# Performance work log

Hardware: AMD Instinct MI355X
Metric: run time of the kernel (lower is better)

Reference implementation:

```python
import jax, jax.numpy as jnp
import numpy as np

N_EXPERTS = 8
D_IN = 1024
D_OUT = 1024
BATCH = 4096


def setup_inputs() -> dict:
    key = jax.random.key(0)
    k_x, k_w, k_b, k_a = jax.random.split(key, 4)
    xs = jax.random.normal(k_x, (BATCH, D_IN), dtype=jnp.float32)
    mxs = jnp.arange(BATCH, dtype=jnp.int32)  # opaque per-sample metadata, passed through
    actions = jax.random.randint(k_a, (BATCH,), 0, N_EXPERTS, dtype=jnp.int64)
    # Expert parameters: each submodule is Linear(D_IN -> D_OUT)
    W = jax.random.normal(k_w, (N_EXPERTS, D_OUT, D_IN), dtype=jnp.float32) / np.sqrt(D_IN)
    b = jax.random.normal(k_b, (N_EXPERTS, D_OUT), dtype=jnp.float32) * 0.01
    return {"xs": xs, "mxs": mxs, "actions": actions, "W": W, "b": b}


def reference(xs, mxs, actions, W, b):
    # Original: per-sample python loop y_i = submodule[actions[i]](x_i); cat along batch.
    # Vectorized: compute all experts densely (E small), then select per-sample row.
    y_all = jnp.einsum("bj,eij->bei", xs, W) + b[None, :, :]  # [B, E, D_OUT]
    ys = jnp.take_along_axis(y_all, actions[:, None, None].astype(jnp.int32), axis=1)
    ys = jnp.squeeze(ys, axis=1)  # [B, D_OUT]
    return (ys, mxs, actions)
```

## Files before the change

### kernel.cpp

```cpp
#include <hip/hip_runtime.h>

#define BATCH 4096
#define D_IN 1024
#define D_OUT 1024
#define N_EXPERTS 8

#define TK 32
#define MAX_TILES 71
#define MAX_TILES_128 39

#define WS_PERM    0
#define WS_STARTS  4096
#define WS_TILE_E  4112
#define WS_TILE_M  4200
#define WS_NTILES  4288

#define WS_XHI_OFF   32768
#define WS_XLO_OFF   (32768 + 8388608)
#define WS_WHI_OFF   (32768 + 2*8388608)
#define WS_WLO_OFF   (32768 + 2*8388608 + 16777216)
#define WS_NEEDED    (32768 + 2*8388608 + 2*16777216)

typedef __attribute__((ext_vector_type(8))) short short8;
typedef __attribute__((ext_vector_type(4))) float f32x4;

__device__ __forceinline__ void cvt8(const float4 a, const float4 b,
                                     short8& h, short8& l) {
    float f[8] = {a.x, a.y, a.z, a.w, b.x, b.y, b.z, b.w};
#pragma unroll
    for (int i = 0; i < 8; ++i) {
        const unsigned u = __float_as_uint(f[i]);
        h[i] = (short)(u >> 16);
        const float r = f[i] - __uint_as_float(u & 0xffff0000u);
        l[i] = (short)(__float_as_uint(r) >> 16);
    }
}

__global__ __launch_bounds__(256) void prep_kernel(
    const int* __restrict__ actions, const int* __restrict__ mxs,
    const float* __restrict__ xs, const float* __restrict__ W,
    int* __restrict__ ws,
    short* __restrict__ XhiP, short* __restrict__ XloP,
    short* __restrict__ WhiP, short* __restrict__ WloP,
    float* __restrict__ out, int meta_mode, int tm_tile)
{
    const int bid = blockIdx.x;
    const int t = threadIdx.x;

    if (bid == 0) {
        __shared__ int chunkoff[64][N_EXPERTS];
        const int lane = t & 63;
        const int wave = t >> 6;

        for (int it = 0; it < 16; ++it) {
            const int c = wave * 16 + it;
            const int a = actions[c * 64 + lane];
            int myc = 0;
#pragma unroll
            for (int e = 0; e < N_EXPERTS; ++e) {
                const unsigned long long me = __ballot(a == e);
                if (lane == e) myc = (int)__popcll(me);
            }
            if (lane < N_EXPERTS) chunkoff[c][lane] = myc;
        }
        __syncthreads();

        if (wave == 0) {
            int cc0 = chunkoff[lane][0], cc1 = chunkoff[lane][1];
            int cc2 = chunkoff[lane][2], cc3 = chunkoff[lane][3];
            int cc4 = chunkoff[lane][4], cc5 = chunkoff[lane][5];
            int cc6 = chunkoff[lane][6], cc7 = chunkoff[lane][7];
            int tot0, tot1, tot2, tot3, tot4, tot5, tot6, tot7;
            int ex0, ex1, ex2, ex3, ex4, ex5, ex6, ex7;
#define SCAN1(CC, TOT, EX) do {                                   \
            int v = CC;                                           \
            _Pragma("unroll")                                     \
            for (int d = 1; d < 64; d <<= 1) {                    \
                const int u = __shfl_up(v, d, 64);                \
                if (lane >= d) v += u;                            \
            }                                                     \
            TOT = __shfl(v, 63, 64);                              \
            EX = v - CC;                                          \
        } while (0)
            SCAN1(cc0, tot0, ex0); SCAN1(cc1, tot1, ex1);
            SCAN1(cc2, tot2, ex2); SCAN1(cc3, tot3, ex3);
            SCAN1(cc4, tot4, ex4); SCAN1(cc5, tot5, ex5);
            SCAN1(cc6, tot6, ex6); SCAN1(cc7, tot7, ex7);
#undef SCAN1
            const int b0 = 0;
            const int b1 = b0 + tot0, b2 = b1 + tot1, b3 = b2 + tot2;
            const int b4 = b3 + tot3, b5 = b4 + tot4, b6 = b5 + tot5;
            const int b7 = b6 + tot6;
            chunkoff[lane][0] = b0 + ex0; chunkoff[lane][1] = b1 + ex1;
            chunkoff[lane][2] = b2 + ex2; chunkoff[lane][3] = b3 + ex3;
            chunkoff[lane][4] = b4 + ex4; chunkoff[lane][5] = b5 + ex5;
            chunkoff[lane][6] = b6 + ex6; chunkoff[lane][7] = b7 + ex7;
            if (lane == 0) {
                ws[WS_STARTS + 0] = b0; ws[WS_STARTS + 1] = b1;
                ws[WS_STARTS + 2] = b2; ws[WS_STARTS + 3] = b3;
                ws[WS_STARTS + 4] = b4; ws[WS_STARTS + 5] = b5;
                ws[WS_STARTS + 6] = b6; ws[WS_STARTS + 7] = b7;
                ws[WS_STARTS + 8] = BATCH;
                int nt = 0;
                int tots[8] = {tot0, tot1, tot2, tot3, tot4, tot5, tot6, tot7};
#pragma unroll
                for (int e = 0; e < N_EXPERTS; ++e)
                    for (int m0 = 0; m0 < tots[e]; m0 += tm_tile) {
                        ws[WS_TILE_E + nt] = e;
                        ws[WS_TILE_M + nt] = m0;
                        ++nt;
                    }
                ws[WS_NTILES] = nt;
            }
        }
        __syncthreads();

        for (int it = 0; it < 16; ++it) {
            const int c = wave * 16 + it;
            const int i = c * 64 + lane;
            const int a = actions[i];
            unsigned long long msel = 0;
#pragma unroll
            for (int e = 0; e < N_EXPERTS; ++e) {
                const unsigned long long me = __ballot(a == e);
                if (a == e) msel = me;
            }
            const int rank = (int)__popcll(msel & ((1ull << lane) - 1ull));
            const int pos = chunkoff[c][a] + rank;
            ws[WS_PERM + pos] = i;
        }
        return;
    }

    if (bid <= 16) {
        const int i = (bid - 1) * 256 + t;
        if (meta_mode == 2) {
            out[BATCH * D_OUT + i] = (float)mxs[i];
            long long* a64 = (long long*)(out + BATCH * D_OUT + BATCH);
            a64[i] = (long long)actions[i];
        } else if (meta_mode == 1) {
            out[BATCH * D_OUT + i] = (float)mxs[i];
            out[BATCH * D_OUT + BATCH + i] = (float)actions[i];
        }
        return;
    }

    const int g = (bid - 17) * 256 + t;
    if (g < 1048576) {
        const int slot = g & 63;
        const int i2   = (g >> 6) & 7;
        const int blk  = g >> 9;
        const int nt   = blk & 7;
        const int kt   = (blk >> 3) & 31;
        const int e    = blk >> 8;
        const int c    = slot & 15;
        const int j    = slot >> 4;
        const int n    = nt * 128 + i2 * 16 + c;
        const float* p = W + ((size_t)(e << 10) + n) * D_IN + kt * 32 + j * 8;
        const float4 f0 = *(const float4*)p;
        const float4 f1 = *(const float4*)(p + 4);
        short8 h, l;
        cvt8(f0, f1, h, l);
        *(short8*)(WhiP + (size_t)g * 8) = h;
        *(short8*)(WloP + (size_t)g * 8) = l;
    } else {
        const int g2 = g - 1048576;
        const float* p = xs + (size_t)g2 * 8;
        const float4 f0 = *(const float4*)p;
        const float4 f1 = *(const float4*)(p + 4);
        short8 h, l;
        cvt8(f0, f1, h, l);
        *(short8*)(XhiP + (size_t)g2 * 8) = h;
        *(short8*)(XloP + (size_t)g2 * 8) = l;
    }
}

#define TM5 128
#define TN5 128

__global__ __launch_bounds__(512) void moe_gemm_pc(
    const short* __restrict__ Xhi, const short* __restrict__ Xlo,
    const short* __restrict__ Whi, const short* __restrict__ Wlo,
    const float* __restrict__ bias, const int* __restrict__ ws,
    float* __restrict__ out)
{
    const int wid = blockIdx.x;
    const int xcd = wid & 7;
    const int j5  = wid >> 3;
    const int nsl = j5 & 7;
    const int tix = (j5 >> 3) * 8 + xcd;
    if (tix >= ws[WS_NTILES]) return;
    const int e   = ws[WS_TILE_E + tix];
    const int m0  = ws[WS_TILE_M + tix];
    const int s0  = ws[WS_STARTS + e];
    const int cnt = ws[WS_STARTS + e + 1] - s0;
    const int n0  = nsl * TN5;

    __shared__ short Ahi[4][8 * 512];
    __shared__ short Alo[4][8 * 512];
    __shared__ short Bhi[4][8 * 512];
    __shared__ short Blo[4][8 * 512];
    __shared__ int   rows_s[TM5];

    const int t = threadIdx.x;
    if (t < TM5) {
        const int r = m0 + t;
        rows_s[t] = (r < cnt) ? ws[WS_PERM + s0 + r] : -1;
    }
    __syncthreads();

    const int lane = t & 63;
    const int wave = t >> 6;
    const int wm = (wave >> 1) * 32;
    const int wn = (wave & 1) * 64;

    const float zf = 0.f;
    f32x4 acc[2][4];
#pragma unroll
    for (int mi = 0; mi < 2; ++mi)
#pragma unroll
        for (int nj = 0; nj < 4; ++nj)
            acc[mi][nj] = (f32x4){zf, zf, zf, zf};

    const int arow0 = rows_s[wave * 16 + (lane & 15)];
    const int arow  = arow0 < 0 ? 0 : arow0;
    const short* aSrcHi = Xhi + (size_t)arow * D_IN + (lane >> 4) * 8;
    const short* aSrcLo = Xlo + (size_t)arow * D_IN + (lane >> 4) * 8;

    const size_t wBase = ((size_t)e * 256 + (size_t)nsl) * 4096;
    const size_t bo = (size_t)wave * 512 + lane * 8;

#define STAGE(KT, BUF) do {                                                    \
        const int _kt = (KT);                                                  \
        __builtin_amdgcn_global_load_lds(                                      \
            (const __attribute__((address_space(1))) void*)(aSrcHi + _kt * 32),\
            (__attribute__((address_space(3))) void*)&Ahi[BUF][wave * 512],    \
            16, 0, 0);                                                         \
        __builtin_amdgcn_global_load_lds(                                      \
            (const __attribute__((address_space(1))) void*)(aSrcLo + _kt * 32),\
            (__attribute__((address_space(3))) void*)&Alo[BUF][wave * 512],    \
            16, 0, 0);                                                         \
        {                                                                      \
            const size_t _wo = wBase + (size_t)_kt * 32768;                    \
            __builtin_amdgcn_global_load_lds(                                  \
                (const __attribute__((address_space(1))) void*)(Whi + _wo + bo), \
                (__attribute__((address_space(3))) void*)&Bhi[BUF][wave * 512],\
                16, 0, 0);                                                     \
            __builtin_amdgcn_global_load_lds(                                  \
                (const __attribute__((address_space(1))) void*)(Wlo + _wo + bo), \
                (__attribute__((address_space(3))) void*)&Blo[BUF][wave * 512],\
                16, 0, 0);                                                     \
        }                                                                      \
    } while (0)

    const int rds = lane * 8;

#define FRAG_MFMA(BUF) do {                                                  \
        short8 ah[2], al[2], bh[4], bl[4];                                   \
        _Pragma("unroll")                                                    \
        for (int i2 = 0; i2 < 2; ++i2) {                                     \
            const int aoff = ((wm >> 4) + i2) * 512 + rds;                   \
            ah[i2] = *(const short8*)&Ahi[BUF][aoff];                        \
            al[i2] = *(const short8*)&Alo[BUF][aoff];                        \
        }                                                                    \
        _Pragma("unroll")                                                    \
        for (int i2 = 0; i2 < 4; ++i2) {                                     \
            const int boff = ((wn >> 4) + i2) * 512 + rds;                   \
            bh[i2] = *(const short8*)&Bhi[BUF][boff];                        \
            bl[i2] = *(const short8*)&Blo[BUF][boff];                        \
        }                                                                    \
        _Pragma("unroll")                                                    \
        for (int mi = 0; mi < 2; ++mi)                                       \
            _Pragma("unroll")                                                \
            for (int nj = 0; nj < 4; ++nj) {                                 \
                acc[mi][nj] = __builtin_amdgcn_mfma_f32_16x16x32_bf16(ah[mi], bh[nj], acc[mi][nj], 0, 0, 0); \
                acc[mi][nj] = __builtin_amdgcn_mfma_f32_16x16x32_bf16(ah[mi], bl[nj], acc[mi][nj], 0, 0, 0); \
                acc[mi][nj] = __builtin_amdgcn_mfma_f32_16x16x32_bf16(al[mi], bh[nj], acc[mi][nj], 0, 0, 0); \
            }                                                                \
    } while (0)

#define WAIT8_BAR() asm volatile("s_waitcnt vmcnt(8) lgkmcnt(0)\n\ts_barrier" ::: "memory")
#define WAIT4_BAR() asm volatile("s_waitcnt vmcnt(4) lgkmcnt(0)\n\ts_barrier" ::: "memory")
#define WAIT0_BAR() asm volatile("s_waitcnt vmcnt(0) lgkmcnt(0)\n\ts_barrier" ::: "memory")

    STAGE(0, 0);
    STAGE(1, 1);
    STAGE(2, 2);

    int kt = 3;
#pragma unroll 1
    for (int i = 0; i < 7; ++i) {
        WAIT8_BAR(); STAGE(kt,     3); FRAG_MFMA(0);
        WAIT8_BAR(); STAGE(kt + 1, 0); FRAG_MFMA(1);
        WAIT8_BAR(); STAGE(kt + 2, 1); FRAG_MFMA(2);
        WAIT8_BAR(); STAGE(kt + 3, 2); FRAG_MFMA(3);
        kt += 4;
    }
    WAIT8_BAR(); STAGE(31, 3); FRAG_MFMA(0);
    WAIT8_BAR(); FRAG_MFMA(1);
    WAIT4_BAR(); FRAG_MFMA(2);
    WAIT0_BAR(); FRAG_MFMA(3);

#undef STAGE
#undef FRAG_MFMA
#undef WAIT8_BAR
#undef WAIT4_BAR
#undef WAIT0_BAR

    const int cl = lane & 15;
    const int qd = lane >> 4;
    float bv[4];
#pragma unroll
    for (int nj = 0; nj < 4; ++nj)
        bv[nj] = bias[e * D_OUT + n0 + wn + nj * 16 + cl];
#pragma unroll
    for (int mi = 0; mi < 2; ++mi) {
#pragma unroll
        for (int reg = 0; reg < 4; ++reg) {
            const int mloc = wm + mi * 16 + qd * 4 + reg;
            const int r = rows_s[mloc];
            if (r >= 0) {
                float* orow = out + (size_t)r * D_OUT + n0 + wn + cl;
#pragma unroll
                for (int nj = 0; nj < 4; ++nj)
                    orow[nj * 16] = acc[mi][nj][reg] + bv[nj];
            }
        }
    }
}

#define TMF 64
#define TNF 128

__global__ __launch_bounds__(256) void moe_gemm_fb(
    const float* __restrict__ xs, const float* __restrict__ W,
    const float* __restrict__ bias, const int* __restrict__ ws,
    float* __restrict__ out)
{
    const int tix = blockIdx.y;
    if (tix >= ws[WS_NTILES]) return;
    const int e   = ws[WS_TILE_E + tix];
    const int m0  = ws[WS_TILE_M + tix];
    const int s0  = ws[WS_STARTS + e];
    const int cnt = ws[WS_STARTS + e + 1] - s0;
    const int n0  = blockIdx.x * TNF;

    __shared__ short Ahi[2][TMF * TK];
    __shared__ short Alo[2][TMF * TK];
    __shared__ short Bhi[2][TNF * TK];
    __shared__ short Blo[2][TNF * TK];
    __shared__ int   rows_s[TMF];

    const int t = threadIdx.x;
    if (t < TMF) {
        const int r = m0 + t;
        rows_s[t] = (r < cnt) ? ws[WS_PERM + s0 + r] : -1;
    }
    __syncthreads();

    const int lane = t & 63;
    const int wave = t >> 6;
    const int wm = (wave & 1) * 32;
    const int wn = (wave >> 1) * 64;

    const float zf = 0.f;
    f32x4 acc[2][4];
#pragma unroll
    for (int mi = 0; mi < 2; ++mi)
#pragma unroll
        for (int nj = 0; nj < 4; ++nj)
            acc[mi][nj] = (f32x4){zf, zf, zf, zf};

    const float* Wb = W + (size_t)e * (D_OUT * (size_t)D_IN) + (size_t)n0 * D_IN;

    const int j  = t & 3;
    const int rr = t >> 2;

    const int arow = rows_s[rr];
    const float* aptr = (arow >= 0) ? (xs + (size_t)arow * D_IN + j * 8) : nullptr;

    const int slotA   = (j * 16 + (rr & 15)) ^ (j << 1);
    const int aoff_st = (rr >> 4) * 512 + slotA * 8;
    const int boff0   = aoff_st;
    const int boff1   = aoff_st + 4 * 512;

    const float* qb0 = Wb + (size_t)rr * D_IN + j * 8;
    const float* qb1 = Wb + (size_t)(64 + rr) * D_IN + j * 8;

    const int rds = (lane ^ ((lane >> 4) << 1)) * 8;

#define LOAD_SET(A0, A1, B0, B1, B2, B3, KOFF) do {                          \
        const int _k = (KOFF);                                               \
        if (aptr) {                                                          \
            A0 = *(const float4*)(aptr + _k);                                \
            A1 = *(const float4*)(aptr + _k + 4);                            \
        }                                                                    \
        B0 = *(const float4*)(qb0 + _k); B1 = *(const float4*)(qb0 + _k + 4);\
        B2 = *(const float4*)(qb1 + _k); B3 = *(const float4*)(qb1 + _k + 4);\
    } while (0)

#define CVT_STORE_SET(A0, A1, B0, B1, B2, B3, BUF) do {                      \
        short8 _h, _l;                                                       \
        cvt8(A0, A1, _h, _l);                                                \
        *(short8*)&Ahi[BUF][aoff_st] = _h; *(short8*)&Alo[BUF][aoff_st] = _l;\
        cvt8(B0, B1, _h, _l);                                                \
        *(short8*)&Bhi[BUF][boff0] = _h;   *(short8*)&Blo[BUF][boff0] = _l;  \
        cvt8(B2, B3, _h, _l);                                                \
        *(short8*)&Bhi[BUF][boff1] = _h;   *(short8*)&Blo[BUF][boff1] = _l;  \
    } while (0)

#define FRAG_MFMA(BUF) do {                                                  \
        short8 ah[2], al[2], bh[4], bl[4];                                   \
        _Pragma("unroll")                                                    \
        for (int i2 = 0; i2 < 2; ++i2) {                                     \
            const int aoff = ((wm >> 4) + i2) * 512 + rds;                   \
            ah[i2] = *(const short8*)&Ahi[BUF][aoff];                        \
            al[i2] = *(const short8*)&Alo[BUF][aoff];                        \
        }                                                                    \
        _Pragma("unroll")                                                    \
        for (int i2 = 0; i2 < 4; ++i2) {                                     \
            const int boff = ((wn >> 4) + i2) * 512 + rds;                   \
            bh[i2] = *(const short8*)&Bhi[BUF][boff];                        \
            bl[i2] = *(const short8*)&Blo[BUF][boff];                        \
        }                                                                    \
        _Pragma("unroll")                                                    \
        for (int mi = 0; mi < 2; ++mi)                                       \
            _Pragma("unroll")                                                \
            for (int nj = 0; nj < 4; ++nj) {                                 \
                acc[mi][nj] = __builtin_amdgcn_mfma_f32_16x16x32_bf16(ah[mi], bh[nj], acc[mi][nj], 0, 0, 0); \
                acc[mi][nj] = __builtin_amdgcn_mfma_f32_16x16x32_bf16(ah[mi], bl[nj], acc[mi][nj], 0, 0, 0); \
                acc[mi][nj] = __builtin_amdgcn_mfma_f32_16x16x32_bf16(al[mi], bh[nj], acc[mi][nj], 0, 0, 0); \
            }                                                                \
    } while (0)

#define PIPE_BARRIER() asm volatile("s_waitcnt lgkmcnt(0)\n\ts_barrier" ::: "memory")

    float4 ax0 = make_float4(0.f, 0.f, 0.f, 0.f), ax1 = ax0;
    float4 bx0, bx1, bx2, bx3;
    float4 ay0 = make_float4(0.f, 0.f, 0.f, 0.f), ay1 = ay0;
    float4 by0, by1, by2, by3;

    LOAD_SET(ax0, ax1, bx0, bx1, bx2, bx3, 0);
    CVT_STORE_SET(ax0, ax1, bx0, bx1, bx2, bx3, 0);
    LOAD_SET(ax0, ax1, bx0, bx1, bx2, bx3, TK);
    PIPE_BARRIER();

    int ke = 2 * TK;
#pragma unroll 1
    for (int i = 0; i < 15; ++i) {
        {
            LOAD_SET(ay0, ay1, by0, by1, by2, by3, ke);
            FRAG_MFMA(0);
            CVT_STORE_SET(ax0, ax1, bx0, bx1, bx2, bx3, 1);
            PIPE_BARRIER();
        }
        {
            LOAD_SET(ax0, ax1, bx0, bx1, bx2, bx3, ke + TK);
            FRAG_MFMA(1);
            CVT_STORE_SET(ay0, ay1, by0, by1, by2, by3, 0);
            PIPE_BARRIER();
        }
        ke += 2 * TK;
    }
    {
        FRAG_MFMA(0);
        CVT_STORE_SET(ax0, ax1, bx0, bx1, bx2, bx3, 1);
        PIPE_BARRIER();
    }
    {
        FRAG_MFMA(1);
    }

#undef LOAD_SET
#undef CVT_STORE_SET
#undef FRAG_MFMA
#undef PIPE_BARRIER

    const int cl = lane & 15;
    const int qd = lane >> 4;
    float bv[4];
#pragma unroll
    for (int nj = 0; nj < 4; ++nj)
        bv[nj] = bias[e * D_OUT + n0 + wn + nj * 16 + cl];
#pragma unroll
    for (int mi = 0; mi < 2; ++mi) {
#pragma unroll
        for (int reg = 0; reg < 4; ++reg) {
            const int mloc = wm + mi * 16 + qd * 4 + reg;
            const int r = rows_s[mloc];
            if (r >= 0) {
                float* orow = out + (size_t)r * D_OUT + n0 + wn + cl;
#pragma unroll
                for (int nj = 0; nj < 4; ++nj)
                    orow[nj * 16] = acc[mi][nj][reg] + bv[nj];
            }
        }
    }
}

extern "C" void kernel_launch(void* const* d_in, const int* in_sizes, int n_in,
                              void* d_out, int out_size, void* d_ws, size_t ws_size,
                              hipStream_t stream) {
    const float* xs      = (const float*)d_in[0];
    const int*   mxs     = (const int*)d_in[1];
    const int*   actions = (const int*)d_in[2];
    const float* W       = (const float*)d_in[3];
    const float* bias    = (const float*)d_in[4];
    float* out = (float*)d_out;
    int*   ws  = (int*)d_ws;
    char*  wsb = (char*)d_ws;

    short* XhiP = (short*)(wsb + WS_XHI_OFF);
    short* XloP = (short*)(wsb + WS_XLO_OFF);
    short* WhiP = (short*)(wsb + WS_WHI_OFF);
    short* WloP = (short*)(wsb + WS_WLO_OFF);

    const int metaOff = BATCH * D_OUT;
    const int meta_mode = (out_size >= metaOff + 3 * BATCH) ? 2
                        : (out_size >= metaOff + 2 * BATCH) ? 1 : 0;

    const bool big = ws_size >= (size_t)WS_NEEDED;
    const int prep_blocks = big ? (17 + 6144) : 17;
    const int tm_tile = big ? TM5 : TMF;

    prep_kernel<<<prep_blocks, 256, 0, stream>>>(
        actions, mxs, xs, W, ws, XhiP, XloP, WhiP, WloP, out, meta_mode, tm_tile);

    if (big) {
        moe_gemm_pc<<<8 * (MAX_TILES_128 + 1), 512, 0, stream>>>(
            XhiP, XloP, WhiP, WloP, bias, ws, out);
    } else {
        dim3 grid(D_OUT / TNF, MAX_TILES, 1);
        moe_gemm_fb<<<grid, 256, 0, stream>>>(xs, W, bias, ws, out);
    }
}
```

Baseline: 160.3 us.

## Replace LDS-staged 128x128 expert GEMM with direct-register 32-row strip kernel

Replaces the 512-thread LDS-pipelined kernel (128x128 tiles, global_load_lds staging into a 4-stage buffer) with a 256-thread kernel that loads pre-packed bf16 hi/lo fragments straight from global memory into registers, with double-buffered register sets and no LDS or barriers. Tiles become 32-row strips by 256 columns, and jobs are split contiguously across XCDs to balance work. This cuts barrier and LDS traffic and reduces padding waste with smaller row tiles. The cost is less data reuse: each wave refetches its own A rows and B fragments from L2, which raises global memory traffic.

```diff
diff --git a/kernel.cpp b/kernel.cpp
--- a/kernel.cpp
+++ b/kernel.cpp
@@ -7,13 +7,14 @@
 
 #define TK 32
 #define MAX_TILES 71
-#define MAX_TILES_128 39
+#define TSTRIP 32
+#define MAX_STRIPS 136
 
 #define WS_PERM    0
 #define WS_STARTS  4096
 #define WS_TILE_E  4112
-#define WS_TILE_M  4200
-#define WS_NTILES  4288
+#define WS_TILE_M  4280
+#define WS_NTILES  4448
 
 #define WS_XHI_OFF   32768
 #define WS_XLO_OFF   (32768 + 8388608)
@@ -175,35 +176,156 @@
     }
 }
 
-#define TM5 128
-#define TN5 128
-
-__global__ __launch_bounds__(512) void moe_gemm_pc(
+__global__ __launch_bounds__(256, 2) void moe_gemm_dr(
     const short* __restrict__ Xhi, const short* __restrict__ Xlo,
     const short* __restrict__ Whi, const short* __restrict__ Wlo,
     const float* __restrict__ bias, const int* __restrict__ ws,
     float* __restrict__ out)
 {
+    __shared__ int rows_s[TSTRIP];
+
+    const int nstrips = ws[WS_NTILES];
+    const int njobs = nstrips * 4;
     const int wid = blockIdx.x;
     const int xcd = wid & 7;
-    const int j5  = wid >> 3;
-    const int nsl = j5 & 7;
-    const int tix = (j5 >> 3) * 8 + xcd;
+    const int lin = wid >> 3;
+    const int q8 = njobs >> 3, r8 = njobs & 7;
+    const int mylen = (xcd < r8) ? (q8 + 1) : q8;
+    if (lin >= mylen) return;
+    const int job = ((xcd < r8) ? xcd * (q8 + 1)
+                                : r8 * (q8 + 1) + (xcd - r8) * q8) + lin;
+    const int q = job / nstrips;
+    const int s = job - q * nstrips;
+
+    const int e   = ws[WS_TILE_E + s];
+    const int m0  = ws[WS_TILE_M + s];
+    const int s0  = ws[WS_STARTS + e];
+    const int cnt = ws[WS_STARTS + e + 1] - s0;
+
+    const int t = threadIdx.x;
+    if (t < TSTRIP) {
+        const int r = m0 + t;
+        rows_s[t] = (r < cnt) ? ws[WS_PERM + s0 + r] : -1;
+    }
+    __syncthreads();
+
+    const int lane = t & 63;
+    const int wave = t >> 6;
+    const int n0 = q * 256 + wave * 64;
+
+    const float zf = 0.f;
+    f32x4 acc[2][4];
+#pragma unroll
+    for (int mi = 0; mi < 2; ++mi)
+#pragma unroll
+        for (int nj = 0; nj < 4; ++nj)
+            acc[mi][nj] = (f32x4){zf, zf, zf, zf};
+
+    const int fr = lane & 15;
+    const int jo = lane >> 4;
+    int r0 = rows_s[fr];      if (r0 < 0) r0 = 0;
+    int r1 = rows_s[16 + fr]; if (r1 < 0) r1 = 0;
+    const short* aH0 = Xhi + (size_t)r0 * D_IN + jo * 8;
+    const short* aH1 = Xhi + (size_t)r1 * D_IN + jo * 8;
+    const short* aL0 = Xlo + (size_t)r0 * D_IN + jo * 8;
+    const short* aL1 = Xlo + (size_t)r1 * D_IN + jo * 8;
+
+    const size_t wtb = ((size_t)e * 32) * 64 + (size_t)(n0 >> 4);
+    const short* bH = Whi + wtb * 512 + lane * 8;
+    const short* bL = Wlo + wtb * 512 + lane * 8;
+
+#define LOADSET(AH0, AH1, AL0, AL1, B0h, B1h, B2h, B3h, B0l, B1l, B2l, B3l, KT) do { \
+        const int _o = (KT) * 32;                                             \
+        AH0 = *(const short8*)(aH0 + _o);                                     \
+        AH1 = *(const short8*)(aH1 + _o);                                     \
+        AL0 = *(const short8*)(aL0 + _o);                                     \
+        AL1 = *(const short8*)(aL1 + _o);                                     \
+        const short* _bh = bH + (size_t)(KT) * 32768;                         \
+        const short* _bl = bL + (size_t)(KT) * 32768;                         \
+        B0h = *(const short8*)(_bh);        B1h = *(const short8*)(_bh + 512);\
+        B2h = *(const short8*)(_bh + 1024); B3h = *(const short8*)(_bh + 1536);\
+        B0l = *(const short8*)(_bl);        B1l = *(const short8*)(_bl + 512);\
+        B2l = *(const short8*)(_bl + 1024); B3l = *(const short8*)(_bl + 1536);\
+    } while (0)
+
+#define MFMA1(MI, NJ, AH, AL, BH, BL) do {                                   \
+        acc[MI][NJ] = __builtin_amdgcn_mfma_f32_16x16x32_bf16(AH, BH, acc[MI][NJ], 0, 0, 0); \
+        acc[MI][NJ] = __builtin_amdgcn_mfma_f32_16x16x32_bf16(AH, BL, acc[MI][NJ], 0, 0, 0); \
+        acc[MI][NJ] = __builtin_amdgcn_mfma_f32_16x16x32_bf16(AL, BH, acc[MI][NJ], 0, 0, 0); \
+    } while (0)
+
+#define MFMASET(AH0, AH1, AL0, AL1, B0h, B1h, B2h, B3h, B0l, B1l, B2l, B3l) do { \
+        MFMA1(0, 0, AH0, AL0, B0h, B0l); MFMA1(0, 1, AH0, AL0, B1h, B1l);    \
+        MFMA1(0, 2, AH0, AL0, B2h, B2l); MFMA1(0, 3, AH0, AL0, B3h, B3l);    \
+        MFMA1(1, 0, AH1, AL1, B0h, B0l); MFMA1(1, 1, AH1, AL1, B1h, B1l);    \
+        MFMA1(1, 2, AH1, AL1, B2h, B2l); MFMA1(1, 3, AH1, AL1, B3h, B3l);    \
+    } while (0)
+
+    short8 xah0, xah1, xal0, xal1, xb0h, xb1h, xb2h, xb3h, xb0l, xb1l, xb2l, xb3l;
+    short8 yah0, yah1, yal0, yal1, yb0h, yb1h, yb2h, yb3h, yb0l, yb1l, yb2l, yb3l;
+
+    LOADSET(xah0, xah1, xal0, xal1, xb0h, xb1h, xb2h, xb3h, xb0l, xb1l, xb2l, xb3l, 0);
+#pragma unroll 1
+    for (int i = 0; i < 15; ++i) {
+        LOADSET(yah0, yah1, yal0, yal1, yb0h, yb1h, yb2h, yb3h, yb0l, yb1l, yb2l, yb3l, 2 * i + 1);
+        MFMASET(xah0, xah1, xal0, xal1, xb0h, xb1h, xb2h, xb3h, xb0l, xb1l, xb2l, xb3l);
+        LOADSET(xah0, xah1, xal0, xal1, xb0h, xb1h, xb2h, xb3h, xb0l, xb1l, xb2l, xb3l, 2 * i + 2);
+        MFMASET(yah0, yah1, yal0, yal1, yb0h, yb1h, yb2h, yb3h, yb0l, yb1l, yb2l, yb3l);
+    }
+    LOADSET(yah0, yah1, yal0, yal1, yb0h, yb1h, yb2h, yb3h, yb0l, yb1l, yb2l, yb3l, 31);
+    MFMASET(xah0, xah1, xal0, xal1, xb0h, xb1h, xb2h, xb3h, xb0l, xb1l, xb2l, xb3l);
+    MFMASET(yah0, yah1, yal0, yal1, yb0h, yb1h, yb2h, yb3h, yb0l, yb1l, yb2l, yb3l);
+
+#undef LOADSET
+#undef MFMA1
+#undef MFMASET
+
+    const int cl = lane & 15;
+    const int qd = lane >> 4;
+    float bv[4];
+#pragma unroll
+    for (int nj = 0; nj < 4; ++nj)
+        bv[nj] = bias[e * D_OUT + n0 + nj * 16 + cl];
+#pragma unroll
+    for (int mi = 0; mi < 2; ++mi) {
+#pragma unroll
+        for (int reg = 0; reg < 4; ++reg) {
+            const int mloc = mi * 16 + qd * 4 + reg;
+            const int r = rows_s[mloc];
+            if (r >= 0) {
+                float* orow = out + (size_t)r * D_OUT + n0 + cl;
+#pragma unroll
+                for (int nj = 0; nj < 4; ++nj)
+                    orow[nj * 16] = acc[mi][nj][reg] + bv[nj];
+            }
+        }
+    }
+}
+
+#define TMF 64
+#define TNF 128
+
+__global__ __launch_bounds__(256) void moe_gemm_fb(
+    const float* __restrict__ xs, const float* __restrict__ W,
+    const float* __restrict__ bias, const int* __restrict__ ws,
+    float* __restrict__ out)
+{
+    const int tix = blockIdx.y;
     if (tix >= ws[WS_NTILES]) return;
     const int e   = ws[WS_TILE_E + tix];
     const int m0  = ws[WS_TILE_M + tix];
     const int s0  = ws[WS_STARTS + e];
     const int cnt = ws[WS_STARTS + e + 1] - s0;
-    const int n0  = nsl * TN5;
-
-    __shared__ short Ahi[4][8 * 512];
-    __shared__ short Alo[4][8 * 512];
-    __shared__ short Bhi[4][8 * 512];
-    __shared__ short Blo[4][8 * 512];
-    __shared__ int   rows_s[TM5];
+    const int n0  = blockIdx.x * TNF;
+
+    __shared__ short Ahi[2][TMF * TK];
+    __shared__ short Alo[2][TMF * TK];
+    __shared__ short Bhi[2][TNF * TK];
+    __shared__ short Blo[2][TNF * TK];
+    __shared__ int   rows_s[TMF];
 
     const int t = threadIdx.x;
-    if (t < TM5) {
+    if (t < TMF) {
         const int r = m0 + t;
         rows_s[t] = (r < cnt) ? ws[WS_PERM + s0 + r] : -1;
     }
@@ -211,8 +333,8 @@
 
     const int lane = t & 63;
     const int wave = t >> 6;
-    const int wm = (wave >> 1) * 32;
-    const int wn = (wave & 1) * 64;
+    const int wm = (wave & 1) * 32;
+    const int wn = (wave >> 1) * 64;
 
     const float zf = 0.f;
     f32x4 acc[2][4];
@@ -222,38 +344,43 @@
         for (int nj = 0; nj < 4; ++nj)
             acc[mi][nj] = (f32x4){zf, zf, zf, zf};
 
-    const int arow0 = rows_s[wave * 16 + (lane & 15)];
-    const int arow  = arow0 < 0 ? 0 : arow0;
-    const short* aSrcHi = Xhi + (size_t)arow * D_IN + (lane >> 4) * 8;
-    const short* aSrcLo = Xlo + (size_t)arow * D_IN + (lane >> 4) * 8;
-
-    const size_t wBase = ((size_t)e * 256 + (size_t)nsl) * 4096;
-    const size_t bo = (size_t)wave * 512 + lane * 8;
-
-#define STAGE(KT, BUF) do {                                                    \
-        const int _kt = (KT);                                                  \
-        __builtin_amdgcn_global_load_lds(                                      \
-            (const __attribute__((address_space(1))) void*)(aSrcHi + _kt * 32),\
-            (__attribute__((address_space(3))) void*)&Ahi[BUF][wave * 512],    \
-            16, 0, 0);                                                         \
-        __builtin_amdgcn_global_load_lds(                                      \
-            (const __attribute__((address_space(1))) void*)(aSrcLo + _kt * 32),\
-            (__attribute__((address_space(3))) void*)&Alo[BUF][wave * 512],    \
-            16, 0, 0);                                                         \
-        {                                                                      \
-            const size_t _wo = wBase + (size_t)_kt * 32768;                    \
-            __builtin_amdgcn_global_load_lds(                                  \
-                (const __attribute__((address_space(1))) void*)(Whi + _wo + bo), \
-                (__attribute__((address_space(3))) void*)&Bhi[BUF][wave * 512],\
-                16, 0, 0);                                                     \
-            __builtin_amdgcn_global_load_lds(                                  \
-                (const __attribute__((address_space(1))) void*)(Wlo + _wo + bo), \
-                (__attribute__((address_space(3))) void*)&Blo[BUF][wave * 512],\
-                16, 0, 0);                                                     \
-        }                                                                      \
+    const float* Wb = W + (size_t)e * (D_OUT * (size_t)D_IN) + (size_t)n0 * D_IN;
+
+    const int j  = t & 3;
+    const int rr = t >> 2;
+
+    const int arow = rows_s[rr];
+    const float* aptr = (arow >= 0) ? (xs + (size_t)arow * D_IN + j * 8) : nullptr;
+
+    const int slotA   = (j * 16 + (rr & 15)) ^ (j << 1);
+    const int aoff_st = (rr >> 4) * 512 + slotA * 8;
+    const int boff0   = aoff_st;
+    const int boff1   = aoff_st + 4 * 512;
+
+    const float* qb0 = Wb + (size_t)rr * D_IN + j * 8;
+    const float* qb1 = Wb + (size_t)(64 + rr) * D_IN + j * 8;
+
+    const int rds = (lane ^ ((lane >> 4) << 1)) * 8;
+
+#define LOAD_SET(A0, A1, B0, B1, B2, B3, KOFF) do {                          \
+        const int _k = (KOFF);                                               \
+        if (aptr) {                                                          \
+            A0 = *(const float4*)(aptr + _k);                                \
+            A1 = *(const float4*)(aptr + _k + 4);                            \
+        }                                                                    \
+        B0 = *(const float4*)(qb0 + _k); B1 = *(const float4*)(qb0 + _k + 4);\
+        B2 = *(const float4*)(qb1 + _k); B3 = *(const float4*)(qb1 + _k + 4);\
     } while (0)
 
-    const int rds = lane * 8;
+#define CVT_STORE_SET(A0, A1, B0, B1, B2, B3, BUF) do {                      \
+        short8 _h, _l;                                                       \
+        cvt8(A0, A1, _h, _l);                                                \
+        *(short8*)&Ahi[BUF][aoff_st] = _h; *(short8*)&Alo[BUF][aoff_st] = _l;\
+        cvt8(B0, B1, _h, _l);                                                \
+        *(short8*)&Bhi[BUF][boff0] = _h;   *(short8*)&Blo[BUF][boff0] = _l;  \
+        cvt8(B2, B3, _h, _l);                                                \
+        *(short8*)&Bhi[BUF][boff1] = _h;   *(short8*)&Blo[BUF][boff1] = _l;  \
+    } while (0)
 
 #define FRAG_MFMA(BUF) do {                                                  \
         short8 ah[2], al[2], bh[4], bl[4];                                   \
@@ -279,160 +406,6 @@
             }                                                                \
     } while (0)
 
-#define WAIT8_BAR() asm volatile("s_waitcnt vmcnt(8) lgkmcnt(0)\n\ts_barrier" ::: "memory")
-#define WAIT4_BAR() asm volatile("s_waitcnt vmcnt(4) lgkmcnt(0)\n\ts_barrier" ::: "memory")
-#define WAIT0_BAR() asm volatile("s_waitcnt vmcnt(0) lgkmcnt(0)\n\ts_barrier" ::: "memory")
-
-    STAGE(0, 0);
-    STAGE(1, 1);
-    STAGE(2, 2);
-
-    int kt = 3;
-#pragma unroll 1
-    for (int i = 0; i < 7; ++i) {
-        WAIT8_BAR(); STAGE(kt,     3); FRAG_MFMA(0);
-        WAIT8_BAR(); STAGE(kt + 1, 0); FRAG_MFMA(1);
-        WAIT8_BAR(); STAGE(kt + 2, 1); FRAG_MFMA(2);
-        WAIT8_BAR(); STAGE(kt + 3, 2); FRAG_MFMA(3);
-        kt += 4;
-    }
-    WAIT8_BAR(); STAGE(31, 3); FRAG_MFMA(0);
-    WAIT8_BAR(); FRAG_MFMA(1);
-    WAIT4_BAR(); FRAG_MFMA(2);
-    WAIT0_BAR(); FRAG_MFMA(3);
-
-#undef STAGE
-#undef FRAG_MFMA
-#undef WAIT8_BAR
-#undef WAIT4_BAR
-#undef WAIT0_BAR
-
-    const int cl = lane & 15;
-    const int qd = lane >> 4;
-    float bv[4];
-#pragma unroll
-    for (int nj = 0; nj < 4; ++nj)
-        bv[nj] = bias[e * D_OUT + n0 + wn + nj * 16 + cl];
-#pragma unroll
-    for (int mi = 0; mi < 2; ++mi) {
-#pragma unroll
-        for (int reg = 0; reg < 4; ++reg) {
-            const int mloc = wm + mi * 16 + qd * 4 + reg;
-            const int r = rows_s[mloc];
-            if (r >= 0) {
-                float* orow = out + (size_t)r * D_OUT + n0 + wn + cl;
-#pragma unroll
-                for (int nj = 0; nj < 4; ++nj)
-                    orow[nj * 16] = acc[mi][nj][reg] + bv[nj];
-            }
-        }
-    }
-}
-
-#define TMF 64
-#define TNF 128
-
-__global__ __launch_bounds__(256) void moe_gemm_fb(
-    const float* __restrict__ xs, const float* __restrict__ W,
-    const float* __restrict__ bias, const int* __restrict__ ws,
-    float* __restrict__ out)
-{
-    const int tix = blockIdx.y;
-    if (tix >= ws[WS_NTILES]) return;
-    const int e   = ws[WS_TILE_E + tix];
-    const int m0  = ws[WS_TILE_M + tix];
-    const int s0  = ws[WS_STARTS + e];
-    const int cnt = ws[WS_STARTS + e + 1] - s0;
-    const int n0  = blockIdx.x * TNF;
-
-    __shared__ short Ahi[2][TMF * TK];
-    __shared__ short Alo[2][TMF * TK];
-    __shared__ short Bhi[2][TNF * TK];
-    __shared__ short Blo[2][TNF * TK];
-    __shared__ int   rows_s[TMF];
-
-    const int t = threadIdx.x;
-    if (t < TMF) {
-        const int r = m0 + t;
-        rows_s[t] = (r < cnt) ? ws[WS_PERM + s0 + r] : -1;
-    }
-    __syncthreads();
-
-    const int lane = t & 63;
-    const int wave = t >> 6;
-    const int wm = (wave & 1) * 32;
-    const int wn = (wave >> 1) * 64;
-
-    const float zf = 0.f;
-    f32x4 acc[2][4];
-#pragma unroll
-    for (int mi = 0; mi < 2; ++mi)
-#pragma unroll
-        for (int nj = 0; nj < 4; ++nj)
-            acc[mi][nj] = (f32x4){zf, zf, zf, zf};
-
-    const float* Wb = W + (size_t)e * (D_OUT * (size_t)D_IN) + (size_t)n0 * D_IN;
-
-    const int j  = t & 3;
-    const int rr = t >> 2;
-
-    const int arow = rows_s[rr];
-    const float* aptr = (arow >= 0) ? (xs + (size_t)arow * D_IN + j * 8) : nullptr;
-
-    const int slotA   = (j * 16 + (rr & 15)) ^ (j << 1);
-    const int aoff_st = (rr >> 4) * 512 + slotA * 8;
-    const int boff0   = aoff_st;
-    const int boff1   = aoff_st + 4 * 512;
-
-    const float* qb0 = Wb + (size_t)rr * D_IN + j * 8;
-    const float* qb1 = Wb + (size_t)(64 + rr) * D_IN + j * 8;
-
-    const int rds = (lane ^ ((lane >> 4) << 1)) * 8;
-
-#define LOAD_SET(A0, A1, B0, B1, B2, B3, KOFF) do {                          \
-        const int _k = (KOFF);                                               \
-        if (aptr) {                                                          \
-            A0 = *(const float4*)(aptr + _k);                                \
-            A1 = *(const float4*)(aptr + _k + 4);                            \
-        }                                                                    \
-        B0 = *(const float4*)(qb0 + _k); B1 = *(const float4*)(qb0 + _k + 4);\
-        B2 = *(const float4*)(qb1 + _k); B3 = *(const float4*)(qb1 + _k + 4);\
-    } while (0)
-
-#define CVT_STORE_SET(A0, A1, B0, B1, B2, B3, BUF) do {                      \
-        short8 _h, _l;                                                       \
-        cvt8(A0, A1, _h, _l);                                                \
-        *(short8*)&Ahi[BUF][aoff_st] = _h; *(short8*)&Alo[BUF][aoff_st] = _l;\
-        cvt8(B0, B1, _h, _l);                                                \
-        *(short8*)&Bhi[BUF][boff0] = _h;   *(short8*)&Blo[BUF][boff0] = _l;  \
-        cvt8(B2, B3, _h, _l);                                                \
-        *(short8*)&Bhi[BUF][boff1] = _h;   *(short8*)&Blo[BUF][boff1] = _l;  \
-    } while (0)
-
-#define FRAG_MFMA(BUF) do {                                                  \
-        short8 ah[2], al[2], bh[4], bl[4];                                   \
-        _Pragma("unroll")                                                    \
-        for (int i2 = 0; i2 < 2; ++i2) {                                     \
-            const int aoff = ((wm >> 4) + i2) * 512 + rds;                   \
-            ah[i2] = *(const short8*)&Ahi[BUF][aoff];                        \
-            al[i2] = *(const short8*)&Alo[BUF][aoff];                        \
-        }                                                                    \
-        _Pragma("unroll")                                                    \
-        for (int i2 = 0; i2 < 4; ++i2) {                                     \
-            const int boff = ((wn >> 4) + i2) * 512 + rds;                   \
-            bh[i2] = *(const short8*)&Bhi[BUF][boff];                        \
-            bl[i2] = *(const short8*)&Blo[BUF][boff];                        \
-        }                                                                    \
-        _Pragma("unroll")                                                    \
-        for (int mi = 0; mi < 2; ++mi)                                       \
-            _Pragma("unroll")                                                \
-            for (int nj = 0; nj < 4; ++nj) {                                 \
-                acc[mi][nj] = __builtin_amdgcn_mfma_f32_16x16x32_bf16(ah[mi], bh[nj], acc[mi][nj], 0, 0, 0); \
-                acc[mi][nj] = __builtin_amdgcn_mfma_f32_16x16x32_bf16(ah[mi], bl[nj], acc[mi][nj], 0, 0, 0); \
-                acc[mi][nj] = __builtin_amdgcn_mfma_f32_16x16x32_bf16(al[mi], bh[nj], acc[mi][nj], 0, 0, 0); \
-            }                                                                \
-    } while (0)
-
 #define PIPE_BARRIER() asm volatile("s_waitcnt lgkmcnt(0)\n\ts_barrier" ::: "memory")
 
     float4 ax0 = make_float4(0.f, 0.f, 0.f, 0.f), ax1 = ax0;
@@ -521,13 +494,13 @@
 
     const bool big = ws_size >= (size_t)WS_NEEDED;
     const int prep_blocks = big ? (17 + 6144) : 17;
-    const int tm_tile = big ? TM5 : TMF;
+    const int tm_tile = big ? TSTRIP : TMF;
 
     prep_kernel<<<prep_blocks, 256, 0, stream>>>(
         actions, mxs, xs, W, ws, XhiP, XloP, WhiP, WloP, out, meta_mode, tm_tile);
 
     if (big) {
-        moe_gemm_pc<<<8 * (MAX_TILES_128 + 1), 512, 0, stream>>>(
+        moe_gemm_dr<<<4 * MAX_STRIPS, 256, 0, stream>>>(
             XhiP, XloP, WhiP, WloP, bias, ws, out);
     } else {
         dim3 grid(D_OUT / TNF, MAX_TILES, 1);
```

Result: slower. 176.0 us (+9.8%).

## Load gathered A fragments directly into registers, stage only weights through LDS

Applied to the files above, without the earlier changes.

The A-operand (gathered input rows, hi/lo bf16 split) is now loaded straight from global memory into registers with double-buffered register sets, and only the weight tiles go through async global-to-LDS copies. This removes the A-side LDS buffers and the LDS reads for A fragments, halving shared memory use and cutting LDS traffic. Launch bounds now request 4 blocks per SM, and the workspace tile-table offsets are widened. The trade-offs are higher register pressure, uncoalesced per-row global loads for A, and a barrier placed inside each compute step.

```diff
diff --git a/kernel.cpp b/kernel.cpp
--- a/kernel.cpp
+++ b/kernel.cpp
@@ -12,8 +12,8 @@
 #define WS_PERM    0
 #define WS_STARTS  4096
 #define WS_TILE_E  4112
-#define WS_TILE_M  4200
-#define WS_NTILES  4288
+#define WS_TILE_M  4280
+#define WS_NTILES  4448
 
 #define WS_XHI_OFF   32768
 #define WS_XLO_OFF   (32768 + 8388608)
@@ -178,7 +178,7 @@
 #define TM5 128
 #define TN5 128
 
-__global__ __launch_bounds__(512) void moe_gemm_pc(
+__global__ __launch_bounds__(512, 4) void moe_gemm_pc(
     const short* __restrict__ Xhi, const short* __restrict__ Xlo,
     const short* __restrict__ Whi, const short* __restrict__ Wlo,
     const float* __restrict__ bias, const int* __restrict__ ws,
@@ -196,8 +196,6 @@
     const int cnt = ws[WS_STARTS + e + 1] - s0;
     const int n0  = nsl * TN5;
 
-    __shared__ short Ahi[4][8 * 512];
-    __shared__ short Alo[4][8 * 512];
     __shared__ short Bhi[4][8 * 512];
     __shared__ short Blo[4][8 * 512];
     __shared__ int   rows_s[TM5];
@@ -222,38 +220,195 @@
         for (int nj = 0; nj < 4; ++nj)
             acc[mi][nj] = (f32x4){zf, zf, zf, zf};
 
-    const int arow0 = rows_s[wave * 16 + (lane & 15)];
-    const int arow  = arow0 < 0 ? 0 : arow0;
-    const short* aSrcHi = Xhi + (size_t)arow * D_IN + (lane >> 4) * 8;
-    const short* aSrcLo = Xlo + (size_t)arow * D_IN + (lane >> 4) * 8;
+    const int fr = lane & 15;
+    const int jo = lane >> 4;
+    int r0 = rows_s[wm + fr];       if (r0 < 0) r0 = 0;
+    int r1 = rows_s[wm + 16 + fr];  if (r1 < 0) r1 = 0;
+    const short* aH0 = Xhi + (size_t)r0 * D_IN + jo * 8;
+    const short* aH1 = Xhi + (size_t)r1 * D_IN + jo * 8;
+    const short* aL0 = Xlo + (size_t)r0 * D_IN + jo * 8;
+    const short* aL1 = Xlo + (size_t)r1 * D_IN + jo * 8;
 
     const size_t wBase = ((size_t)e * 256 + (size_t)nsl) * 4096;
     const size_t bo = (size_t)wave * 512 + lane * 8;
 
+    short8 Xh0, Xh1, Xl0, Xl1, Yh0, Yh1, Yl0, Yl1;
+
+#define ALOAD(P, KT) do {                                                     \
+        const int _o = (KT) * 32;                                             \
+        P##h0 = *(const short8*)(aH0 + _o);                                   \
+        P##h1 = *(const short8*)(aH1 + _o);                                   \
+        P##l0 = *(const short8*)(aL0 + _o);                                   \
+        P##l1 = *(const short8*)(aL1 + _o);                                   \
+    } while (0)
+
+#define AFENCE() asm volatile("" ::: "memory")
+
 #define STAGE(KT, BUF) do {                                                    \
-        const int _kt = (KT);                                                  \
+        const size_t _wo = wBase + (size_t)(KT) * 32768;                       \
         __builtin_amdgcn_global_load_lds(                                      \
-            (const __attribute__((address_space(1))) void*)(aSrcHi + _kt * 32),\
-            (__attribute__((address_space(3))) void*)&Ahi[BUF][wave * 512],    \
+            (const __attribute__((address_space(1))) void*)(Whi + _wo + bo),   \
+            (__attribute__((address_space(3))) void*)&Bhi[BUF][wave * 512],    \
             16, 0, 0);                                                         \
         __builtin_amdgcn_global_load_lds(                                      \
-            (const __attribute__((address_space(1))) void*)(aSrcLo + _kt * 32),\
-            (__attribute__((address_space(3))) void*)&Alo[BUF][wave * 512],    \
+            (const __attribute__((address_space(1))) void*)(Wlo + _wo + bo),   \
+            (__attribute__((address_space(3))) void*)&Blo[BUF][wave * 512],    \
             16, 0, 0);                                                         \
-        {                                                                      \
-            const size_t _wo = wBase + (size_t)_kt * 32768;                    \
-            __builtin_amdgcn_global_load_lds(                                  \
-                (const __attribute__((address_space(1))) void*)(Whi + _wo + bo), \
-                (__attribute__((address_space(3))) void*)&Bhi[BUF][wave * 512],\
-                16, 0, 0);                                                     \
-            __builtin_amdgcn_global_load_lds(                                  \
-                (const __attribute__((address_space(1))) void*)(Wlo + _wo + bo), \
-                (__attribute__((address_space(3))) void*)&Blo[BUF][wave * 512],\
-                16, 0, 0);                                                     \
-        }                                                                      \
     } while (0)
 
+#define WAITB(N) asm volatile("s_waitcnt vmcnt(" #N ")\n\ts_barrier" ::: "memory")
+
     const int rds = lane * 8;
+
+#define COMPUTE(BUF, P) do {                                                 \
+        short8 bh[4], bl[4];                                                 \
+        _Pragma("unroll")                                                    \
+        for (int i2 = 0; i2 < 4; ++i2) {                                     \
+            const int boff = ((wn >> 4) + i2) * 512 + rds;                   \
+            bh[i2] = *(const short8*)&Bhi[BUF][boff];                        \
+            bl[i2] = *(const short8*)&Blo[BUF][boff];                        \
+        }                                                                    \
+        asm volatile("s_waitcnt lgkmcnt(0)\n\ts_barrier" ::: "memory");      \
+        __builtin_amdgcn_sched_barrier(0);                                   \
+        _Pragma("unroll")                                                    \
+        for (int nj = 0; nj < 4; ++nj) {                                     \
+            acc[0][nj] = __builtin_amdgcn_mfma_f32_16x16x32_bf16(P##h0, bh[nj], acc[0][nj], 0, 0, 0); \
+            acc[0][nj] = __builtin_amdgcn_mfma_f32_16x16x32_bf16(P##h0, bl[nj], acc[0][nj], 0, 0, 0); \
+            acc[0][nj] = __builtin_amdgcn_mfma_f32_16x16x32_bf16(P##l0, bh[nj], acc[0][nj], 0, 0, 0); \
+            acc[1][nj] = __builtin_amdgcn_mfma_f32_16x16x32_bf16(P##h1, bh[nj], acc[1][nj], 0, 0, 0); \
+            acc[1][nj] = __builtin_amdgcn_mfma_f32_16x16x32_bf16(P##h1, bl[nj], acc[1][nj], 0, 0, 0); \
+            acc[1][nj] = __builtin_amdgcn_mfma_f32_16x16x32_bf16(P##l1, bh[nj], acc[1][nj], 0, 0, 0); \
+        }                                                                    \
+    } while (0)
+
+    ALOAD(X, 0);
+    AFENCE();
+    STAGE(0, 0); STAGE(1, 1); STAGE(2, 2);
+    ALOAD(Y, 1);
+    AFENCE();
+    STAGE(3, 3);
+    WAITB(6);
+    COMPUTE(0, X);
+
+#pragma unroll 1
+    for (int i = 0; i < 7; ++i) {
+        const int k = 1 + 4 * i;
+        ALOAD(X, k + 1); AFENCE(); STAGE(k + 3, 0); WAITB(8); COMPUTE(1, Y);
+        ALOAD(Y, k + 2); AFENCE(); STAGE(k + 4, 1); WAITB(8); COMPUTE(2, X);
+        ALOAD(X, k + 3); AFENCE(); STAGE(k + 5, 2); WAITB(8); COMPUTE(3, Y);
+        ALOAD(Y, k + 4); AFENCE(); STAGE(k + 6, 3); WAITB(8); COMPUTE(0, X);
+    }
+    ALOAD(X, 30); AFENCE(); WAITB(6); COMPUTE(1, Y);
+    ALOAD(Y, 31); AFENCE(); WAITB(4); COMPUTE(2, X);
+    WAITB(0);                COMPUTE(3, Y);
+
+#undef ALOAD
+#undef AFENCE
+#undef STAGE
+#undef WAITB
+#undef COMPUTE
+
+    const int cl = lane & 15;
+    const int qd = lane >> 4;
+    float bv[4];
+#pragma unroll
+    for (int nj = 0; nj < 4; ++nj)
+        bv[nj] = bias[e * D_OUT + n0 + wn + nj * 16 + cl];
+#pragma unroll
+    for (int mi = 0; mi < 2; ++mi) {
+#pragma unroll
+        for (int reg = 0; reg < 4; ++reg) {
+            const int mloc = wm + mi * 16 + qd * 4 + reg;
+            const int r = rows_s[mloc];
+            if (r >= 0) {
+                float* orow = out + (size_t)r * D_OUT + n0 + wn + cl;
+#pragma unroll
+                for (int nj = 0; nj < 4; ++nj)
+                    orow[nj * 16] = acc[mi][nj][reg] + bv[nj];
+            }
+        }
+    }
+}
+
+#define TMF 64
+#define TNF 128
+
+__global__ __launch_bounds__(256) void moe_gemm_fb(
+    const float* __restrict__ xs, const float* __restrict__ W,
+    const float* __restrict__ bias, const int* __restrict__ ws,
+    float* __restrict__ out)
+{
+    const int tix = blockIdx.y;
+    if (tix >= ws[WS_NTILES]) return;
+    const int e   = ws[WS_TILE_E + tix];
+    const int m0  = ws[WS_TILE_M + tix];
+    const int s0  = ws[WS_STARTS + e];
+    const int cnt = ws[WS_STARTS + e + 1] - s0;
+    const int n0  = blockIdx.x * TNF;
+
+    __shared__ short Ahi[2][TMF * TK];
+    __shared__ short Alo[2][TMF * TK];
+    __shared__ short Bhi[2][TNF * TK];
+    __shared__ short Blo[2][TNF * TK];
+    __shared__ int   rows_s[TMF];
+
+    const int t = threadIdx.x;
+    if (t < TMF) {
+        const int r = m0 + t;
+        rows_s[t] = (r < cnt) ? ws[WS_PERM + s0 + r] : -1;
+    }
+    __syncthreads();
+
+    const int lane = t & 63;
+    const int wave = t >> 6;
+    const int wm = (wave & 1) * 32;
+    const int wn = (wave >> 1) * 64;
+
+    const float zf = 0.f;
+    f32x4 acc[2][4];
+#pragma unroll
+    for (int mi = 0; mi < 2; ++mi)
+#pragma unroll
+        for (int nj = 0; nj < 4; ++nj)
+            acc[mi][nj] = (f32x4){zf, zf, zf, zf};
+
+    const float* Wb = W + (size_t)e * (D_OUT * (size_t)D_IN) + (size_t)n0 * D_IN;
+
+    const int j  = t & 3;
+    const int rr = t >> 2;
+
+    const int arow = rows_s[rr];
+    const float* aptr = (arow >= 0) ? (xs + (size_t)arow * D_IN + j * 8) : nullptr;
+
+    const int slotA   = (j * 16 + (rr & 15)) ^ (j << 1);
+    const int aoff_st = (rr >> 4) * 512 + slotA * 8;
+    const int boff0   = aoff_st;
+    const int boff1   = aoff_st + 4 * 512;
+
+    const float* qb0 = Wb + (size_t)rr * D_IN + j * 8;
+    const float* qb1 = Wb + (size_t)(64 + rr) * D_IN + j * 8;
+
+    const int rds = (lane ^ ((lane >> 4) << 1)) * 8;
+
+#define LOAD_SET(A0, A1, B0, B1, B2, B3, KOFF) do {                          \
+        const int _k = (KOFF);                                               \
+        if (aptr) {                                                          \
+            A0 = *(const float4*)(aptr + _k);                                \
+            A1 = *(const float4*)(aptr + _k + 4);                            \
+        }                                                                    \
+        B0 = *(const float4*)(qb0 + _k); B1 = *(const float4*)(qb0 + _k + 4);\
+        B2 = *(const float4*)(qb1 + _k); B3 = *(const float4*)(qb1 + _k + 4);\
+    } while (0)
+
+#define CVT_STORE_SET(A0, A1, B0, B1, B2, B3, BUF) do {                      \
+        short8 _h, _l;                                                       \
+        cvt8(A0, A1, _h, _l);                                                \
+        *(short8*)&Ahi[BUF][aoff_st] = _h; *(short8*)&Alo[BUF][aoff_st] = _l;\
+        cvt8(B0, B1, _h, _l);                                                \
+        *(short8*)&Bhi[BUF][boff0] = _h;   *(short8*)&Blo[BUF][boff0] = _l;  \
+        cvt8(B2, B3, _h, _l);                                                \
+        *(short8*)&Bhi[BUF][boff1] = _h;   *(short8*)&Blo[BUF][boff1] = _l;  \
+    } while (0)
 
 #define FRAG_MFMA(BUF) do {                                                  \
         short8 ah[2], al[2], bh[4], bl[4];                                   \
@@ -279,160 +434,6 @@
             }                                                                \
     } while (0)
 
-#define WAIT8_BAR() asm volatile("s_waitcnt vmcnt(8) lgkmcnt(0)\n\ts_barrier" ::: "memory")
-#define WAIT4_BAR() asm volatile("s_waitcnt vmcnt(4) lgkmcnt(0)\n\ts_barrier" ::: "memory")
-#define WAIT0_BAR() asm volatile("s_waitcnt vmcnt(0) lgkmcnt(0)\n\ts_barrier" ::: "memory")
-
-    STAGE(0, 0);
-    STAGE(1, 1);
-    STAGE(2, 2);
-
-    int kt = 3;
-#pragma unroll 1
-    for (int i = 0; i < 7; ++i) {
-        WAIT8_BAR(); STAGE(kt,     3); FRAG_MFMA(0);
-        WAIT8_BAR(); STAGE(kt + 1, 0); FRAG_MFMA(1);
-        WAIT8_BAR(); STAGE(kt + 2, 1); FRAG_MFMA(2);
-        WAIT8_BAR(); STAGE(kt + 3, 2); FRAG_MFMA(3);
-        kt += 4;
-    }
-    WAIT8_BAR(); STAGE(31, 3); FRAG_MFMA(0);
-    WAIT8_BAR(); FRAG_MFMA(1);
-    WAIT4_BAR(); FRAG_MFMA(2);
-    WAIT0_BAR(); FRAG_MFMA(3);
-
-#undef STAGE
-#undef FRAG_MFMA
-#undef WAIT8_BAR
-#undef WAIT4_BAR
-#undef WAIT0_BAR
-
-    const int cl = lane & 15;
-    const int qd = lane >> 4;
-    float bv[4];
-#pragma unroll
-    for (int nj = 0; nj < 4; ++nj)
-        bv[nj] = bias[e * D_OUT + n0 + wn + nj * 16 + cl];
-#pragma unroll
-    for (int mi = 0; mi < 2; ++mi) {
-#pragma unroll
-        for (int reg = 0; reg < 4; ++reg) {
-            const int mloc = wm + mi * 16 + qd * 4 + reg;
-            const int r = rows_s[mloc];
-            if (r >= 0) {
-                float* orow = out + (size_t)r * D_OUT + n0 + wn + cl;
-#pragma unroll
-                for (int nj = 0; nj < 4; ++nj)
-                    orow[nj * 16] = acc[mi][nj][reg] + bv[nj];
-            }
-        }
-    }
-}
-
-#define TMF 64
-#define TNF 128
-
-__global__ __launch_bounds__(256) void moe_gemm_fb(
-    const float* __restrict__ xs, const float* __restrict__ W,
-    const float* __restrict__ bias, const int* __restrict__ ws,
-    float* __restrict__ out)
-{
-    const int tix = blockIdx.y;
-    if (tix >= ws[WS_NTILES]) return;
-    const int e   = ws[WS_TILE_E + tix];
-    const int m0  = ws[WS_TILE_M + tix];
-    const int s0  = ws[WS_STARTS + e];
-    const int cnt = ws[WS_STARTS + e + 1] - s0;
-    const int n0  = blockIdx.x * TNF;
-
-    __shared__ short Ahi[2][TMF * TK];
-    __shared__ short Alo[2][TMF * TK];
-    __shared__ short Bhi[2][TNF * TK];
-    __shared__ short Blo[2][TNF * TK];
-    __shared__ int   rows_s[TMF];
-
-    const int t = threadIdx.x;
-    if (t < TMF) {
-        const int r = m0 + t;
-        rows_s[t] = (r < cnt) ? ws[WS_PERM + s0 + r] : -1;
-    }
-    __syncthreads();
-
-    const int lane = t & 63;
-    const int wave = t >> 6;
-    const int wm = (wave & 1) * 32;
-    const int wn = (wave >> 1) * 64;
-
-    const float zf = 0.f;
-    f32x4 acc[2][4];
-#pragma unroll
-    for (int mi = 0; mi < 2; ++mi)
-#pragma unroll
-        for (int nj = 0; nj < 4; ++nj)
-            acc[mi][nj] = (f32x4){zf, zf, zf, zf};
-
-    const float* Wb = W + (size_t)e * (D_OUT * (size_t)D_IN) + (size_t)n0 * D_IN;
-
-    const int j  = t & 3;
-    const int rr = t >> 2;
-
-    const int arow = rows_s[rr];
-    const float* aptr = (arow >= 0) ? (xs + (size_t)arow * D_IN + j * 8) : nullptr;
-
-    const int slotA   = (j * 16 + (rr & 15)) ^ (j << 1);
-    const int aoff_st = (rr >> 4) * 512 + slotA * 8;
-    const int boff0   = aoff_st;
-    const int boff1   = aoff_st + 4 * 512;
-
-    const float* qb0 = Wb + (size_t)rr * D_IN + j * 8;
-    const float* qb1 = Wb + (size_t)(64 + rr) * D_IN + j * 8;
-
-    const int rds = (lane ^ ((lane >> 4) << 1)) * 8;
-
-#define LOAD_SET(A0, A1, B0, B1, B2, B3, KOFF) do {                          \
-        const int _k = (KOFF);                                               \
-        if (aptr) {                                                          \
-            A0 = *(const float4*)(aptr + _k);                                \
-            A1 = *(const float4*)(aptr + _k + 4);                            \
-        }                                                                    \
-        B0 = *(const float4*)(qb0 + _k); B1 = *(const float4*)(qb0 + _k + 4);\
-        B2 = *(const float4*)(qb1 + _k); B3 = *(const float4*)(qb1 + _k + 4);\
-    } while (0)
-
-#define CVT_STORE_SET(A0, A1, B0, B1, B2, B3, BUF) do {                      \
-        short8 _h, _l;                                                       \
-        cvt8(A0, A1, _h, _l);                                                \
-        *(short8*)&Ahi[BUF][aoff_st] = _h; *(short8*)&Alo[BUF][aoff_st] = _l;\
-        cvt8(B0, B1, _h, _l);                                                \
-        *(short8*)&Bhi[BUF][boff0] = _h;   *(short8*)&Blo[BUF][boff0] = _l;  \
-        cvt8(B2, B3, _h, _l);                                                \
-        *(short8*)&Bhi[BUF][boff1] = _h;   *(short8*)&Blo[BUF][boff1] = _l;  \
-    } while (0)
-
-#define FRAG_MFMA(BUF) do {                                                  \
-        short8 ah[2], al[2], bh[4], bl[4];                                   \
-        _Pragma("unroll")                                                    \
-        for (int i2 = 0; i2 < 2; ++i2) {                                     \
-            const int aoff = ((wm >> 4) + i2) * 512 + rds;                   \
-            ah[i2] = *(const short8*)&Ahi[BUF][aoff];                        \
-            al[i2] = *(const short8*)&Alo[BUF][aoff];                        \
-        }                                                                    \
-        _Pragma("unroll")                                                    \
-        for (int i2 = 0; i2 < 4; ++i2) {                                     \
-            const int boff = ((wn >> 4) + i2) * 512 + rds;                   \
-            bh[i2] = *(const short8*)&Bhi[BUF][boff];                        \
-            bl[i2] = *(const short8*)&Blo[BUF][boff];                        \
-        }                                                                    \
-        _Pragma("unroll")                                                    \
-        for (int mi = 0; mi < 2; ++mi)                                       \
-            _Pragma("unroll")                                                \
-            for (int nj = 0; nj < 4; ++nj) {                                 \
-                acc[mi][nj] = __builtin_amdgcn_mfma_f32_16x16x32_bf16(ah[mi], bh[nj], acc[mi][nj], 0, 0, 0); \
-                acc[mi][nj] = __builtin_amdgcn_mfma_f32_16x16x32_bf16(ah[mi], bl[nj], acc[mi][nj], 0, 0, 0); \
-                acc[mi][nj] = __builtin_amdgcn_mfma_f32_16x16x32_bf16(al[mi], bh[nj], acc[mi][nj], 0, 0, 0); \
-            }                                                                \
-    } while (0)
-
 #define PIPE_BARRIER() asm volatile("s_waitcnt lgkmcnt(0)\n\ts_barrier" ::: "memory")
 
     float4 ax0 = make_float4(0.f, 0.f, 0.f, 0.f), ax1 = ax0;
```

Result: slower. 180.0 us (+12.3%).
